# Performance work log

Measured on AMD Instinct MI355X. Metric: run time of the kernel, lower is better.

Reference implementation:

```python
import jax, jax.numpy as jnp
import numpy as np

D_MODEL, D_FF, R, N_ADAPTERS = 1024, 4096, 8, 4


def setup_inputs() -> dict:
    key = jax.random.key(0)
    ks = jax.random.split(key, 8)
    s1 = 1.0 / np.sqrt(D_MODEL)
    s2 = 1.0 / np.sqrt(D_FF)
    x = jax.random.normal(ks[0], (4, 4096, D_MODEL), dtype=jnp.float32)
    w1 = jax.random.uniform(ks[1], (D_MODEL, D_FF), jnp.float32, -s1, s1)
    b1 = jax.random.uniform(ks[2], (D_FF,), jnp.float32, -s1, s1)
    w2 = jax.random.uniform(ks[3], (D_FF, D_MODEL), jnp.float32, -s2, s2)
    b2 = jax.random.uniform(ks[4], (D_MODEL,), jnp.float32, -s2, s2)
    # stacked adapters: down [A, d_model, r], up [A, r, d_model] (no bias)
    a_down = jax.random.uniform(ks[5], (N_ADAPTERS, D_MODEL, R), jnp.float32, -s1, s1)
    a_up = jax.random.uniform(ks[6], (N_ADAPTERS, R, D_MODEL), jnp.float32, -1.0 / np.sqrt(R), 1.0 / np.sqrt(R))
    return {"x": x, "w1": w1, "b1": b1, "w2": w2, "b2": b2,
            "a_down": a_down, "a_up": a_up, "adapter_idx": 0}


def reference(x, w1, b1, w2, b2, a_down, a_up, adapter_idx):
    # FFN: gelu(x @ w1 + b1) @ w2 + b2  (torch F.gelu default = exact erf form)
    h = jax.nn.gelu(jnp.einsum('bsd,df->bsf', x, w1) + b1, approximate=False)
    out = jnp.einsum('bsf,fd->bsd', h, w2) + b2
    # low-rank adapter residual: (x @ A_down) @ A_up
    lora = jnp.einsum('bsd,dr->bsr', x, a_down[adapter_idx])
    out = out + jnp.einsum('bsr,rd->bsd', lora, a_up[adapter_idx])
    return out
```

## Files before the change

kernel.cpp:

```cpp
#include <hip/hip_runtime.h>
#include <hip/hip_bf16.h>
#include <math.h>

typedef __attribute__((ext_vector_type(4))) float floatx4;
typedef __attribute__((ext_vector_type(8))) __bf16 bfloatx8;
typedef __attribute__((ext_vector_type(8))) unsigned short ushortx8;

static __device__ __forceinline__ unsigned short f2bf(float f) {
  __hip_bfloat16 h = __float2bfloat16(f);
  return *reinterpret_cast<unsigned short*>(&h);
}

static __device__ __forceinline__ void gload16(const void* g, void* l) {
  __builtin_amdgcn_global_load_lds(
      (const __attribute__((address_space(1))) unsigned int*)g,
      (__attribute__((address_space(3))) unsigned int*)l, 16, 0, 0);
}

#define S_BARRIER() __builtin_amdgcn_s_barrier()
#define WAIT_VM(n)  do { asm volatile("s_waitcnt vmcnt(" #n ")" ::: "memory"); __builtin_amdgcn_sched_barrier(0); } while (0)

__global__ __launch_bounds__(256) void transpose_bf16_kernel(const float* __restrict__ in,
                                                             unsigned short* __restrict__ out,
                                                             int rows, int cols) {
  __shared__ float tile[32][33];
  int c0 = blockIdx.x * 32, r0 = blockIdx.y * 32;
  int tx = threadIdx.x, ty = threadIdx.y;
#pragma unroll
  for (int j = 0; j < 32; j += 8)
    tile[ty + j][tx] = in[(size_t)(r0 + ty + j) * cols + c0 + tx];
  __syncthreads();
#pragma unroll
  for (int j = 0; j < 32; j += 8)
    out[(size_t)(c0 + ty + j) * rows + r0 + tx] = f2bf(tile[tx][ty + j]);
}

__global__ __launch_bounds__(256) void lora_mid_convert_kernel(const float* __restrict__ x,
                                                               const float* __restrict__ a_down,
                                                               const int* __restrict__ idxp,
                                                               float* __restrict__ lmid,
                                                               unsigned short* __restrict__ Xb) {
  __shared__ float ad[1024 * 9];
  const float* A = a_down + (size_t)(*idxp) * (1024 * 8);
  int t = threadIdx.x;
  for (int i = t; i < 2048; i += 256) {
    float4 v = ((const float4*)A)[i];
    int row = i >> 1, p = (i & 1) * 4;
    ad[row * 9 + p] = v.x; ad[row * 9 + p + 1] = v.y;
    ad[row * 9 + p + 2] = v.z; ad[row * 9 + p + 3] = v.w;
  }
  __syncthreads();
  int wid = t >> 6, lane = t & 63;
  int row = blockIdx.x * 4 + wid;
  const float4* xr4 = (const float4*)(x + (size_t)row * 1024);
  ushort4* xbr4 = (ushort4*)(Xb + (size_t)row * 1024);
  float acc[8] = {0.f, 0.f, 0.f, 0.f, 0.f, 0.f, 0.f, 0.f};
#pragma unroll
  for (int c = 0; c < 4; ++c) {
    int i4 = c * 64 + lane;
    float4 xv = xr4[i4];
    ushort4 o;
    o.x = f2bf(xv.x); o.y = f2bf(xv.y); o.z = f2bf(xv.z); o.w = f2bf(xv.w);
    xbr4[i4] = o;
    const int kb = i4 * 4;
    const float xs[4] = {xv.x, xv.y, xv.z, xv.w};
#pragma unroll
    for (int j = 0; j < 4; ++j)
#pragma unroll
      for (int r = 0; r < 8; ++r) acc[r] += xs[j] * ad[(kb + j) * 9 + r];
  }
#pragma unroll
  for (int off = 32; off > 0; off >>= 1) {
#pragma unroll
    for (int r = 0; r < 8; ++r) acc[r] += __shfl_xor(acc[r], off);
  }
  if (lane == 0) {
    *(float4*)(lmid + (size_t)row * 8) = make_float4(acc[0], acc[1], acc[2], acc[3]);
    *(float4*)(lmid + (size_t)row * 8 + 4) = make_float4(acc[4], acc[5], acc[6], acc[7]);
  }
}

template <int LD, int NKT>
static __device__ __forceinline__ void gemm_kloop3(const unsigned short* __restrict__ A,
                                                   const unsigned short* __restrict__ B,
                                                   size_t m0, size_t n0, char* smem,
                                                   floatx4 (&acc)[4][4]) {
  const int t = threadIdx.x;
  const int wid = t >> 6, lane = t & 63;
  const int wr = wid >> 1, wc = wid & 1;
  const int lr = lane & 15, kg = lane >> 4;
  const int kgx = kg ^ ((lr >> 1) & 3);
  const int srow = t >> 2, scol = ((t & 3) ^ ((t >> 3) & 3)) * 8;
  const unsigned short* gA0 = A + (m0 + srow) * LD + scol;
  const unsigned short* gA1 = A + (m0 + 64 + srow) * LD + scol;
  const unsigned short* gB0 = B + (n0 + srow) * LD + scol;
  const unsigned short* gB1 = B + (n0 + 64 + srow) * LD + scol;
  const unsigned ldsOff = (unsigned)(wid << 10);

#define STAGE(bufb, ko)                           \
  do {                                            \
    char* lA_ = smem + (bufb) + ldsOff;           \
    char* lB_ = smem + (bufb) + 8192 + ldsOff;    \
    gload16(gA0 + (ko), lA_);                     \
    gload16(gA1 + (ko), lA_ + 4096);              \
    gload16(gB0 + (ko), lB_);                     \
    gload16(gB1 + (ko), lB_ + 4096);              \
  } while (0)

  STAGE(0u, 0);
  STAGE(16384u, 32);
  WAIT_VM(4);
  S_BARRIER();

  unsigned cur = 0u, stg = 32768u;
#pragma unroll 1
  for (int kt = 0; kt < NKT; ++kt) {
    if (kt + 2 < NKT) STAGE(stg, (kt + 2) * 32);
    const unsigned short* As = (const unsigned short*)(smem + cur);
    const unsigned short* Bs = (const unsigned short*)(smem + cur + 8192);
    bfloatx8 af[4], bfv[4];
#pragma unroll
    for (int mi = 0; mi < 4; ++mi)
      af[mi] = *(const bfloatx8*)(As + (wr * 64 + mi * 16 + lr) * 32 + kgx * 8);
#pragma unroll
    for (int ni = 0; ni < 4; ++ni)
      bfv[ni] = *(const bfloatx8*)(Bs + (wc * 64 + ni * 16 + lr) * 32 + kgx * 8);
#pragma unroll
    for (int mi = 0; mi < 4; ++mi) {
#pragma unroll
      for (int ni = 0; ni < 4; ++ni)
        acc[mi][ni] = __builtin_amdgcn_mfma_f32_16x16x32_bf16(af[mi], bfv[ni], acc[mi][ni], 0, 0, 0);
    }
    if (kt + 2 < NKT) { WAIT_VM(4); } else { WAIT_VM(0); }
    S_BARRIER();
    cur = (cur == 32768u) ? 0u : cur + 16384u;
    stg = (stg == 32768u) ? 0u : stg + 16384u;
  }
#undef STAGE
}

template <int LD, int NKT>
static __device__ __forceinline__ void gemm_kloop3w(const unsigned short* __restrict__ A,
                                                    const unsigned short* __restrict__ B,
                                                    size_t m0, size_t n0, char* smem,
                                                    floatx4 (&acc)[4][8]) {
  const int t = threadIdx.x;
  const int wm = t >> 6, lane = t & 63;
  const int lr = lane & 15, kg = lane >> 4;
  const int kgx = kg ^ ((lr >> 1) & 3);
  const int srow = t >> 2, scol = ((t & 3) ^ ((t >> 3) & 3)) * 8;
  const unsigned short* gA = A + (m0 + srow) * LD + scol;
  const unsigned short* gB = B + (n0 + srow) * LD + scol;
  const unsigned ldsW = (unsigned)(wm << 10);

#define STAGE(bufb, ko)                                  \
  do {                                                   \
    char* a_ = smem + (bufb) + ldsW;                     \
    gload16(gA + (ko), a_);                              \
    gload16(gA + (size_t)64 * LD + (ko), a_ + 4096);     \
    gload16(gA + (size_t)128 * LD + (ko), a_ + 8192);    \
    gload16(gA + (size_t)192 * LD + (ko), a_ + 12288);   \
    char* b_ = smem + (bufb) + 16384 + ldsW;             \
    gload16(gB + (ko), b_);                              \
    gload16(gB + (size_t)64 * LD + (ko), b_ + 4096);     \
  } while (0)

  STAGE(0u, 0);
  STAGE(24576u, 32);
  WAIT_VM(6);
  S_BARRIER();

  unsigned cur = 0u, stg = 49152u;
#pragma unroll 1
  for (int kt = 0; kt < NKT; ++kt) {
    if (kt + 2 < NKT) STAGE(stg, (kt + 2) * 32);
    const unsigned short* As = (const unsigned short*)(smem + cur);
    const unsigned short* Bs = (const unsigned short*)(smem + cur + 16384);
    bfloatx8 af[4], bf[8];
#pragma unroll
    for (int mi = 0; mi < 4; ++mi)
      af[mi] = *(const bfloatx8*)(As + (unsigned)(wm * 64 + mi * 16 + lr) * 32 + (unsigned)kgx * 8);
#pragma unroll
    for (int ni = 0; ni < 8; ++ni)
      bf[ni] = *(const bfloatx8*)(Bs + (unsigned)(ni * 16 + lr) * 32 + (unsigned)kgx * 8);
#pragma unroll
    for (int mi = 0; mi < 4; ++mi) {
#pragma unroll
      for (int ni = 0; ni < 8; ++ni)
        acc[mi][ni] = __builtin_amdgcn_mfma_f32_16x16x32_bf16(af[mi], bf[ni], acc[mi][ni], 0, 0, 0);
    }
    if (kt + 2 < NKT) { WAIT_VM(6); } else { WAIT_VM(0); }
    S_BARRIER();
    cur = (cur == 49152u) ? 0u : cur + 24576u;
    stg = (stg == 49152u) ? 0u : stg + 24576u;
  }
#undef STAGE
}

__global__ __launch_bounds__(256, 3) void gemm1_gelu_kernel(const unsigned short* __restrict__ A,
                                                            const unsigned short* __restrict__ B,
                                                            const float* __restrict__ bias,
                                                            unsigned short* __restrict__ H) {
  __shared__ __align__(16) char smem[49152];
  const int t = threadIdx.x;
  const int wid = t >> 6, lane = t & 63;
  const int wr = wid >> 1, wc = wid & 1;
  const int lr = lane & 15, kg = lane >> 4;

  const int bid = blockIdx.x;
  const int xcd = bid & 7, j = bid >> 3;
  const int sq = j >> 6, i = j & 63;
  const int mt = xcd * 16 + (sq & 1) * 8 + (i & 7);
  const int nt = (sq >> 1) * 8 + (i >> 3);
  const size_t m0 = (size_t)mt * 128;
  const size_t n0 = (size_t)nt * 128;

  floatx4 acc[4][4] = {};
  gemm_kloop3<1024, 32>(A, B, m0, n0, smem, acc);

  __syncthreads();
  float* sE = (float*)smem;
  const int row32 = t >> 3, col0 = (t & 7) * 16;
  const int stripe = row32 >> 4, lrow = row32 & 15;
#pragma unroll
  for (int mi = 0; mi < 4; ++mi) {
#pragma unroll
    for (int ni = 0; ni < 4; ++ni) {
#pragma unroll
      for (int r = 0; r < 4; ++r)
        sE[wr * 2048 + (kg * 4 + r) * 128 + wc * 64 + ni * 16 + lr] = acc[mi][ni][r];
    }
    __syncthreads();
    const size_t gm = m0 + stripe * 64 + mi * 16 + lrow;
    const float* src = sE + stripe * 2048 + lrow * 128 + col0;
    alignas(16) unsigned short pk[16];
#pragma unroll
    for (int i2 = 0; i2 < 16; ++i2) {
      float v = src[i2] + bias[n0 + col0 + i2];
      float g = 0.5f * v * (1.0f + erff(v * 0.70710678118654752440f));
      pk[i2] = f2bf(g);
    }
    *(ushortx8*)(H + gm * 4096 + n0 + col0) = *(const ushortx8*)&pk[0];
    *(ushortx8*)(H + gm * 4096 + n0 + col0 + 8) = *(const ushortx8*)&pk[8];
    __syncthreads();
  }
}

__global__ __launch_bounds__(256, 2) void gemm2_out_kernel(const unsigned short* __restrict__ A,
                                                           const unsigned short* __restrict__ B,
                                                           const float* __restrict__ bias,
                                                           const float* __restrict__ lmid,
                                                           const float* __restrict__ a_up,
                                                           const int* __restrict__ idxp,
                                                           float* __restrict__ OUT) {
  extern __shared__ char smem[];
  const int t = threadIdx.x;
  const int wm = t >> 6, lane = t & 63, lr = lane & 15, kg = lane >> 4;

  const int bid = blockIdx.x;
  const int xcd = bid & 7, j = bid >> 3;
  const size_t m0 = (size_t)(xcd * 8 + (j >> 3)) * 256;
  const size_t n0 = (size_t)(j & 7) * 128;

  floatx4 acc[4][8] = {};
  gemm_kloop3w<4096, 128>(A, B, m0, n0, smem, acc);

  __syncthreads();
  float* sE = (float*)smem;
  const float* aup = a_up + (size_t)(*idxp) * 8192;
#pragma unroll
  for (int mi = 0; mi < 4; ++mi) {
#pragma unroll
    for (int ni = 0; ni < 8; ++ni)
#pragma unroll
      for (int r = 0; r < 4; ++r)
        sE[(wm * 16 + kg * 4 + r) * 128 + ni * 16 + lr] = acc[mi][ni][r];
    __syncthreads();
#pragma unroll
    for (int half = 0; half < 2; ++half) {
      const int sr = half * 32 + (t >> 3);
      const int col0 = (t & 7) * 16;
      const size_t gm = m0 + (size_t)(sr >> 4) * 64 + mi * 16 + (sr & 15);
      const int gc = (int)n0 + col0;
      const float* src = sE + sr * 128 + col0;
      alignas(16) float lmv[8];
      *(float4*)&lmv[0] = *(const float4*)(lmid + gm * 8);
      *(float4*)&lmv[4] = *(const float4*)(lmid + gm * 8 + 4);
      alignas(16) float v[16];
#pragma unroll
      for (int i2 = 0; i2 < 16; ++i2) v[i2] = src[i2] + bias[gc + i2];
#pragma unroll
      for (int r = 0; r < 8; ++r) {
        const float lw = lmv[r];
        const float* ar = aup + r * 1024 + gc;
#pragma unroll
        for (int i2 = 0; i2 < 16; ++i2) v[i2] += lw * ar[i2];
      }
#pragma unroll
      for (int i2 = 0; i2 < 16; i2 += 4)
        *(float4*)(OUT + gm * 1024 + gc + i2) = *(const float4*)&v[i2];
    }
    __syncthreads();
  }
}

extern "C" void kernel_launch(void* const* d_in, const int* in_sizes, int n_in,
                              void* d_out, int out_size, void* d_ws, size_t ws_size,
                              hipStream_t stream) {
  const float* x      = (const float*)d_in[0];
  const float* w1     = (const float*)d_in[1];
  const float* b1     = (const float*)d_in[2];
  const float* w2     = (const float*)d_in[3];
  const float* b2     = (const float*)d_in[4];
  const float* a_down = (const float*)d_in[5];
  const float* a_up   = (const float*)d_in[6];
  const int*   idx    = (const int*)d_in[7];
  float* out = (float*)d_out;

  char* ws = (char*)d_ws;
  unsigned short* Xb  = (unsigned short*)(ws);
  unsigned short* W1T = (unsigned short*)(ws + 33554432);
  unsigned short* W2T = (unsigned short*)(ws + 41943040);
  float*          LMID = (float*)(ws + 50331648);
  unsigned short* H   = (unsigned short*)(ws + 50855936);

  (void)hipFuncSetAttribute((const void*)gemm2_out_kernel, hipFuncAttributeMaxDynamicSharedMemorySize, 73728);

  transpose_bf16_kernel<<<dim3(128, 32), dim3(32, 8), 0, stream>>>(w1, W1T, 1024, 4096);
  transpose_bf16_kernel<<<dim3(32, 128), dim3(32, 8), 0, stream>>>(w2, W2T, 4096, 1024);
  lora_mid_convert_kernel<<<4096, 256, 0, stream>>>(x, a_down, idx, LMID, Xb);
  gemm1_gelu_kernel<<<4096, 256, 0, stream>>>(Xb, W1T, b1, H);
  gemm2_out_kernel<<<512, 256, 73728, stream>>>(H, W2T, b2, LMID, a_up, idx, out);
}
```

Measured before the change: 482.9 us.

## Split gemm2 256x128 tile across eight waves instead of four

The second GEMM keeps its 256x128 output tile per block but now uses 512 threads (8 waves), each wave computing 32 rows x 128 columns instead of 64 rows. Staging loads are redistributed so each thread issues 3 global-to-LDS loads per k-step, and the epilogue writes 32 contiguous columns per thread. The aim is more waves per CU to hide memory and LDS latency in the final GEMM. In exchange, each wave gets a lower MFMA-to-LDS-read ratio, since every wave still reads all 8 B fragments.

```diff
diff --git a/kernel.cpp b/kernel.cpp
--- a/kernel.cpp
+++ b/kernel.cpp
@@ -139,64 +139,6 @@
 #undef STAGE
 }
 
-template <int LD, int NKT>
-static __device__ __forceinline__ void gemm_kloop3w(const unsigned short* __restrict__ A,
-                                                    const unsigned short* __restrict__ B,
-                                                    size_t m0, size_t n0, char* smem,
-                                                    floatx4 (&acc)[4][8]) {
-  const int t = threadIdx.x;
-  const int wm = t >> 6, lane = t & 63;
-  const int lr = lane & 15, kg = lane >> 4;
-  const int kgx = kg ^ ((lr >> 1) & 3);
-  const int srow = t >> 2, scol = ((t & 3) ^ ((t >> 3) & 3)) * 8;
-  const unsigned short* gA = A + (m0 + srow) * LD + scol;
-  const unsigned short* gB = B + (n0 + srow) * LD + scol;
-  const unsigned ldsW = (unsigned)(wm << 10);
-
-#define STAGE(bufb, ko)                                  \
-  do {                                                   \
-    char* a_ = smem + (bufb) + ldsW;                     \
-    gload16(gA + (ko), a_);                              \
-    gload16(gA + (size_t)64 * LD + (ko), a_ + 4096);     \
-    gload16(gA + (size_t)128 * LD + (ko), a_ + 8192);    \
-    gload16(gA + (size_t)192 * LD + (ko), a_ + 12288);   \
-    char* b_ = smem + (bufb) + 16384 + ldsW;             \
-    gload16(gB + (ko), b_);                              \
-    gload16(gB + (size_t)64 * LD + (ko), b_ + 4096);     \
-  } while (0)
-
-  STAGE(0u, 0);
-  STAGE(24576u, 32);
-  WAIT_VM(6);
-  S_BARRIER();
-
-  unsigned cur = 0u, stg = 49152u;
-#pragma unroll 1
-  for (int kt = 0; kt < NKT; ++kt) {
-    if (kt + 2 < NKT) STAGE(stg, (kt + 2) * 32);
-    const unsigned short* As = (const unsigned short*)(smem + cur);
-    const unsigned short* Bs = (const unsigned short*)(smem + cur + 16384);
-    bfloatx8 af[4], bf[8];
-#pragma unroll
-    for (int mi = 0; mi < 4; ++mi)
-      af[mi] = *(const bfloatx8*)(As + (unsigned)(wm * 64 + mi * 16 + lr) * 32 + (unsigned)kgx * 8);
-#pragma unroll
-    for (int ni = 0; ni < 8; ++ni)
-      bf[ni] = *(const bfloatx8*)(Bs + (unsigned)(ni * 16 + lr) * 32 + (unsigned)kgx * 8);
-#pragma unroll
-    for (int mi = 0; mi < 4; ++mi) {
-#pragma unroll
-      for (int ni = 0; ni < 8; ++ni)
-        acc[mi][ni] = __builtin_amdgcn_mfma_f32_16x16x32_bf16(af[mi], bf[ni], acc[mi][ni], 0, 0, 0);
-    }
-    if (kt + 2 < NKT) { WAIT_VM(6); } else { WAIT_VM(0); }
-    S_BARRIER();
-    cur = (cur == 49152u) ? 0u : cur + 24576u;
-    stg = (stg == 49152u) ? 0u : stg + 24576u;
-  }
-#undef STAGE
-}
-
 __global__ __launch_bounds__(256, 3) void gemm1_gelu_kernel(const unsigned short* __restrict__ A,
                                                             const unsigned short* __restrict__ B,
                                                             const float* __restrict__ bias,
@@ -246,60 +188,102 @@
   }
 }
 
-__global__ __launch_bounds__(256, 2) void gemm2_out_kernel(const unsigned short* __restrict__ A,
-                                                           const unsigned short* __restrict__ B,
-                                                           const float* __restrict__ bias,
-                                                           const float* __restrict__ lmid,
-                                                           const float* __restrict__ a_up,
-                                                           const int* __restrict__ idxp,
-                                                           float* __restrict__ OUT) {
+__global__ __launch_bounds__(512) void gemm2_out_kernel(const unsigned short* __restrict__ A,
+                                                        const unsigned short* __restrict__ B,
+                                                        const float* __restrict__ bias,
+                                                        const float* __restrict__ lmid,
+                                                        const float* __restrict__ a_up,
+                                                        const int* __restrict__ idxp,
+                                                        float* __restrict__ OUT) {
   extern __shared__ char smem[];
   const int t = threadIdx.x;
-  const int wm = t >> 6, lane = t & 63, lr = lane & 15, kg = lane >> 4;
+  const int w = t >> 6, lane = t & 63, lr = lane & 15, kg = lane >> 4;
+  const int kgx = kg ^ ((lr >> 1) & 3);
+  constexpr int LD = 4096, NKT = 128;
 
   const int bid = blockIdx.x;
   const int xcd = bid & 7, j = bid >> 3;
   const size_t m0 = (size_t)(xcd * 8 + (j >> 3)) * 256;
   const size_t n0 = (size_t)(j & 7) * 128;
 
-  floatx4 acc[4][8] = {};
-  gemm_kloop3w<4096, 128>(A, B, m0, n0, smem, acc);
+  const int sr = w * 16 + ((lane) >> 2);
+  const int scol = ((t & 3) ^ ((sr >> 1) & 3)) * 8;
+  const unsigned short* gA0 = A + (m0 + sr) * LD + scol;
+  const unsigned short* gA1 = A + (m0 + 128 + sr) * LD + scol;
+  const unsigned short* gB = B + (n0 + sr) * LD + scol;
+  const unsigned wOff = (unsigned)(w << 10);
+
+#define STAGE2(bufb, ko)                              \
+  do {                                                \
+    gload16(gA0 + (ko), smem + (bufb) + wOff);        \
+    gload16(gA1 + (ko), smem + (bufb) + 8192 + wOff); \
+    gload16(gB + (ko), smem + (bufb) + 16384 + wOff); \
+  } while (0)
+
+  floatx4 acc[2][8] = {};
+
+  STAGE2(0u, 0);
+  STAGE2(24576u, 32);
+  WAIT_VM(3);
+  S_BARRIER();
+
+  unsigned cur = 0u, stg = 49152u;
+#pragma unroll 1
+  for (int kt = 0; kt < NKT; ++kt) {
+    if (kt + 2 < NKT) STAGE2(stg, (kt + 2) * 32);
+    const unsigned short* As = (const unsigned short*)(smem + cur);
+    const unsigned short* Bs = (const unsigned short*)(smem + cur + 16384);
+    bfloatx8 af[2], bf[8];
+#pragma unroll
+    for (int mi = 0; mi < 2; ++mi)
+      af[mi] = *(const bfloatx8*)(As + (unsigned)(w * 32 + mi * 16 + lr) * 32 + (unsigned)kgx * 8);
+#pragma unroll
+    for (int ni = 0; ni < 8; ++ni)
+      bf[ni] = *(const bfloatx8*)(Bs + (unsigned)(ni * 16 + lr) * 32 + (unsigned)kgx * 8);
+#pragma unroll
+    for (int mi = 0; mi < 2; ++mi) {
+#pragma unroll
+      for (int ni = 0; ni < 8; ++ni)
+        acc[mi][ni] = __builtin_amdgcn_mfma_f32_16x16x32_bf16(af[mi], bf[ni], acc[mi][ni], 0, 0, 0);
+    }
+    if (kt + 2 < NKT) { WAIT_VM(3); } else { WAIT_VM(0); }
+    S_BARRIER();
+    cur = (cur == 49152u) ? 0u : cur + 24576u;
+    stg = (stg == 49152u) ? 0u : stg + 24576u;
+  }
+#undef STAGE2
 
   __syncthreads();
   float* sE = (float*)smem;
   const float* aup = a_up + (size_t)(*idxp) * 8192;
-#pragma unroll
-  for (int mi = 0; mi < 4; ++mi) {
+  const int es = t >> 2, ec0 = (t & 3) * 32;
+#pragma unroll
+  for (int mi = 0; mi < 2; ++mi) {
 #pragma unroll
     for (int ni = 0; ni < 8; ++ni)
 #pragma unroll
       for (int r = 0; r < 4; ++r)
-        sE[(wm * 16 + kg * 4 + r) * 128 + ni * 16 + lr] = acc[mi][ni][r];
+        sE[(w * 16 + kg * 4 + r) * 128 + ni * 16 + lr] = acc[mi][ni][r];
     __syncthreads();
-#pragma unroll
-    for (int half = 0; half < 2; ++half) {
-      const int sr = half * 32 + (t >> 3);
-      const int col0 = (t & 7) * 16;
-      const size_t gm = m0 + (size_t)(sr >> 4) * 64 + mi * 16 + (sr & 15);
-      const int gc = (int)n0 + col0;
-      const float* src = sE + sr * 128 + col0;
-      alignas(16) float lmv[8];
-      *(float4*)&lmv[0] = *(const float4*)(lmid + gm * 8);
-      *(float4*)&lmv[4] = *(const float4*)(lmid + gm * 8 + 4);
-      alignas(16) float v[16];
-#pragma unroll
-      for (int i2 = 0; i2 < 16; ++i2) v[i2] = src[i2] + bias[gc + i2];
-#pragma unroll
-      for (int r = 0; r < 8; ++r) {
-        const float lw = lmv[r];
-        const float* ar = aup + r * 1024 + gc;
-#pragma unroll
-        for (int i2 = 0; i2 < 16; ++i2) v[i2] += lw * ar[i2];
-      }
-#pragma unroll
-      for (int i2 = 0; i2 < 16; i2 += 4)
-        *(float4*)(OUT + gm * 1024 + gc + i2) = *(const float4*)&v[i2];
-    }
+    const size_t gm = m0 + (size_t)(es >> 4) * 32 + mi * 16 + (es & 15);
+    const int gc = (int)n0 + ec0;
+    const float* src = sE + es * 128 + ec0;
+    alignas(16) float lmv[8];
+    *(float4*)&lmv[0] = *(const float4*)(lmid + gm * 8);
+    *(float4*)&lmv[4] = *(const float4*)(lmid + gm * 8 + 4);
+    alignas(16) float v[32];
+#pragma unroll
+    for (int i2 = 0; i2 < 32; ++i2) v[i2] = src[i2] + bias[gc + i2];
+#pragma unroll
+    for (int r = 0; r < 8; ++r) {
+      const float lw = lmv[r];
+      const float* ar = aup + r * 1024 + gc;
+#pragma unroll
+      for (int i2 = 0; i2 < 32; ++i2) v[i2] += lw * ar[i2];
+    }
+#pragma unroll
+    for (int i2 = 0; i2 < 32; i2 += 4)
+      *(float4*)(OUT + gm * 1024 + gc + i2) = *(const float4*)&v[i2];
     __syncthreads();
   }
 }
@@ -330,5 +314,5 @@
   transpose_bf16_kernel<<<dim3(32, 128), dim3(32, 8), 0, stream>>>(w2, W2T, 4096, 1024);
   lora_mid_convert_kernel<<<4096, 256, 0, stream>>>(x, a_down, idx, LMID, Xb);
   gemm1_gelu_kernel<<<4096, 256, 0, stream>>>(Xb, W1T, b1, H);
-  gemm2_out_kernel<<<512, 256, 73728, stream>>>(H, W2T, b2, LMID, a_up, idx, out);
-}
+  gemm2_out_kernel<<<512, 512, 73728, stream>>>(H, W2T, b2, LMID, a_up, idx, out);
+}
```

After: 565.0 us. 1.17x slower.
